# Kernel tuning notes

Measured on AMD Instinct MI355X. Metric: run time of the kernel, lower is better.

## Reference

```python
import jax, jax.numpy as jnp
import numpy as np

N_DRUG, N_DIS, E, D = 10000, 15000, 1048576, 128

def setup_inputs() -> dict:
    key = jax.random.key(0)
    k = jax.random.split(key, 6)
    return {
        "z_drug": jax.random.normal(k[0], (N_DRUG, D), dtype=jnp.float32),
        "z_disease": jax.random.normal(k[1], (N_DIS, D), dtype=jnp.float32),
        "row": jax.random.randint(k[2], (E,), 0, N_DRUG),
        "col": jax.random.randint(k[3], (E,), 0, N_DIS),
        "W1": jax.random.normal(k[4], (2 * D, D), dtype=jnp.float32) * (1.0 / np.sqrt(2 * D)),
        "b1": jnp.zeros((D,), dtype=jnp.float32),
        "W2": jax.random.normal(k[5], (D, 1), dtype=jnp.float32) * (1.0 / np.sqrt(D)),
        "b2": jnp.zeros((1,), dtype=jnp.float32),
    }

def reference(z_drug, z_disease, row, col, W1, b1, W2, b2):
    # gather per-edge embeddings and concatenate: [E, 2D]
    z = jnp.concatenate([z_drug[row], z_disease[col]], axis=-1)
    h = jax.nn.relu(z @ W1 + b1)          # [E, D]
    out = h @ W2 + b2                      # [E, 1]
    return out.reshape(-1)                 # [E]
```

## Files before the change

kernel.cpp:

```cpp
#include <hip/hip_runtime.h>

typedef __attribute__((ext_vector_type(8))) short short8;
typedef __attribute__((ext_vector_type(4))) float floatx4;
typedef _Float16 half8 __attribute__((ext_vector_type(8)));
typedef _Float16 half4 __attribute__((ext_vector_type(4)));
typedef _Float16 half2v __attribute__((ext_vector_type(2)));

static __device__ __forceinline__ unsigned short f2bf(float x) {
    unsigned int u = __builtin_bit_cast(unsigned int, x);
    unsigned int r = (u + 0x7FFFu + ((u >> 16) & 1u)) >> 16;
    return (unsigned short)r;
}

__global__ void prep_w1(const float* __restrict__ W1, unsigned short* __restrict__ w1t,
                        unsigned* __restrict__ gcur) {
    int i = blockIdx.x * 256 + threadIdx.x;
    int n = i >> 8;
    int k = i & 255;
    w1t[n * 256 + k] = f2bf(W1[k * 128 + n]);
    if (i < 16) gcur[i] = 0;
}

__global__ __launch_bounds__(256, 2) void mid_kernel(
    const float* __restrict__ zd, const float* __restrict__ zs,
    const unsigned short* __restrict__ w1t, const float* __restrict__ b1,
    _Float16* __restrict__ ud, _Float16* __restrict__ us,
    int ndrows, int nsrows, int ntd, int nbg,
    const int* __restrict__ row, const int* __restrict__ col,
    unsigned* __restrict__ gcur, unsigned* __restrict__ rcbuf,
    unsigned* __restrict__ eidbuf, int E)
{
    if ((int)blockIdx.x < nbg) {
        const int tid  = threadIdx.x;
        const int lane = tid & 63;
        const int wave = tid >> 6;
        const int wh   = wave >> 1;
        const int we   = wave & 1;
        const int l15  = lane & 15;
        const int quad = lane >> 4;

        const int b = blockIdx.x;
        const bool isD = (b < ntd);
        const float* __restrict__ z = isD ? zd : zs;
        _Float16* __restrict__ u = isD ? ud : us;
        const int nrows = isD ? ndrows : nsrows;
        const int m0    = (isD ? b : b - ntd) * 64;
        const int koff0 = isD ? 0 : 128;

        short8 wfrag[16];
        #pragma unroll
        for (int s = 0; s < 4; ++s)
            #pragma unroll
            for (int mt = 0; mt < 4; ++mt)
                wfrag[s * 4 + mt] = *reinterpret_cast<const short8*>(
                    &w1t[(size_t)(wh * 64 + mt * 16 + l15) * 256 + koff0 + s * 32 + quad * 8]);

        floatx4 acc[2][4];
        #pragma unroll
        for (int mt = 0; mt < 4; ++mt) {
            floatx4 bb = *reinterpret_cast<const floatx4*>(&b1[wh * 64 + mt * 16 + quad * 4]);
            bb *= 0.5f;
            acc[0][mt] = bb;
            acc[1][mt] = bb;
        }

        int rowi[2], rowc[2];
        #pragma unroll
        for (int et = 0; et < 2; ++et) {
            rowi[et] = m0 + we * 32 + et * 16 + l15;
            rowc[et] = rowi[et] < nrows ? rowi[et] : nrows - 1;
        }

        #pragma unroll
        for (int s = 0; s < 4; ++s) {
            short8 bf[2];
            #pragma unroll
            for (int et = 0; et < 2; ++et) {
                const float* src = &z[(size_t)rowc[et] * 128 + s * 32 + quad * 8];
                floatx4 lo = *reinterpret_cast<const floatx4*>(src);
                floatx4 hi = *reinterpret_cast<const floatx4*>(src + 4);
                short8 t;
                t[0] = (short)f2bf(lo[0]); t[1] = (short)f2bf(lo[1]);
                t[2] = (short)f2bf(lo[2]); t[3] = (short)f2bf(lo[3]);
                t[4] = (short)f2bf(hi[0]); t[5] = (short)f2bf(hi[1]);
                t[6] = (short)f2bf(hi[2]); t[7] = (short)f2bf(hi[3]);
                bf[et] = t;
            }
            #pragma unroll
            for (int et = 0; et < 2; ++et)
                #pragma unroll
                for (int mt = 0; mt < 4; ++mt)
                    acc[et][mt] = __builtin_amdgcn_mfma_f32_16x16x32_bf16(
                        wfrag[s * 4 + mt], bf[et], acc[et][mt], 0, 0, 0);
        }

        #pragma unroll
        for (int et = 0; et < 2; ++et) {
            if (rowi[et] < nrows) {
                #pragma unroll
                for (int mt = 0; mt < 4; ++mt) {
                    half4 hv;
                    #pragma unroll
                    for (int rr = 0; rr < 4; ++rr) hv[rr] = (_Float16)acc[et][mt][rr];
                    *reinterpret_cast<half4*>(
                        &u[(size_t)rowi[et] * 128 + wh * 64 + mt * 16 + quad * 4]) = hv;
                }
            }
        }
    } else {
        __shared__ unsigned wl[4][4];
        __shared__ unsigned gb[4];
        const int tid  = threadIdx.x;
        const int lane = tid & 63;
        const int wave = tid >> 6;
        const int sb   = blockIdx.x - nbg;
        const long base = (long)sb * 2048;

        unsigned rc[8], off[8];
        int cls0, cls1, cls2, cls3, cls4, cls5, cls6, cls7;
        unsigned w0 = 0, w1 = 0, w2c = 0, w3 = 0;

        #pragma unroll
        for (int k = 0; k < 8; ++k) {
            long e = base + wave * 512 + k * 64 + lane;
            int r = row[e], c = col[e];
            rc[k] = (unsigned)r | ((unsigned)c << 14);
            int cl = ((r >= 5000) ? 2 : 0) | ((c >= 7500) ? 1 : 0);
            unsigned long long m0 = __ballot(cl == 0);
            unsigned long long m1 = __ballot(cl == 1);
            unsigned long long m2 = __ballot(cl == 2);
            unsigned long long m3 = __ballot(cl == 3);
            unsigned long long mlt = (1ull << lane) - 1ull;
            unsigned long long mc = (cl == 0) ? m0 : (cl == 1) ? m1 : (cl == 2) ? m2 : m3;
            unsigned wb = (cl == 0) ? w0 : (cl == 1) ? w1 : (cl == 2) ? w2c : w3;
            off[k] = wb + (unsigned)__popcll(mc & mlt);
            w0 += (unsigned)__popcll(m0); w1 += (unsigned)__popcll(m1);
            w2c += (unsigned)__popcll(m2); w3 += (unsigned)__popcll(m3);
            switch (k) {
                case 0: cls0 = cl; break; case 1: cls1 = cl; break;
                case 2: cls2 = cl; break; case 3: cls3 = cl; break;
                case 4: cls4 = cl; break; case 5: cls5 = cl; break;
                case 6: cls6 = cl; break; default: cls7 = cl; break;
            }
        }
        if (lane < 4) {
            unsigned wv = (lane == 0) ? w0 : (lane == 1) ? w1 : (lane == 2) ? w2c : w3;
            wl[wave][lane] = wv;
        }
        __syncthreads();
        if (tid < 4) {
            unsigned tot = wl[0][tid] + wl[1][tid] + wl[2][tid] + wl[3][tid];
            gb[tid] = atomicAdd(&gcur[tid], tot);
        }
        __syncthreads();
        unsigned p0 = 0, p1 = 0, p2 = 0, p3 = 0;
        for (int w = 0; w < 4; ++w)
            if (w < wave) { p0 += wl[w][0]; p1 += wl[w][1]; p2 += wl[w][2]; p3 += wl[w][3]; }

        #pragma unroll
        for (int k = 0; k < 8; ++k) {
            long e = base + wave * 512 + k * 64 + lane;
            int cl = (k == 0) ? cls0 : (k == 1) ? cls1 : (k == 2) ? cls2 : (k == 3) ? cls3
                   : (k == 4) ? cls4 : (k == 5) ? cls5 : (k == 6) ? cls6 : cls7;
            unsigned pre = (cl == 0) ? p0 : (cl == 1) ? p1 : (cl == 2) ? p2 : p3;
            unsigned pos = gb[cl] + pre + off[k];
            rcbuf[(size_t)cl * E + pos]  = rc[k];
            eidbuf[(size_t)cl * E + pos] = (unsigned)e;
        }
    }
}

__global__ __launch_bounds__(256, 8) void edge_eval(
    const _Float16* __restrict__ ud, const _Float16* __restrict__ us,
    const unsigned* __restrict__ gcur, const unsigned* __restrict__ rcbuf,
    const unsigned* __restrict__ eidbuf,
    const float* __restrict__ w2, const float* __restrict__ b2,
    float* __restrict__ out, int E)
{
    const int tid  = threadIdx.x;
    const int lane = tid & 63;
    const int wave = tid >> 6;
    const int le   = lane >> 3;
    const int q    = lane & 7;
    const int lslot = wave * 8 + le;

    const int b    = blockIdx.x;
    const int xcd  = b & 7;
    const int cls  = xcd >> 1;
    const int sub  = ((b >> 3) << 1) | (xcd & 1);
    const int NSUB = (int)((gridDim.x >> 3) << 1);

    const unsigned n = gcur[cls];
    const int nch = (int)((n + 31u) >> 5);
    const unsigned* __restrict__ rcb = rcbuf + (size_t)cls * E;
    const unsigned* __restrict__ eib = eidbuf + (size_t)cls * E;

#if __has_builtin(__builtin_amdgcn_fdot2)
    half2v w2h[8];
    #pragma unroll
    for (int i = 0; i < 2; ++i)
        #pragma unroll
        for (int p = 0; p < 4; ++p) {
            half2v t;
            t[0] = (_Float16)w2[i * 64 + q * 8 + 2 * p];
            t[1] = (_Float16)w2[i * 64 + q * 8 + 2 * p + 1];
            w2h[i * 4 + p] = t;
        }
#else
    float w2r[16];
    #pragma unroll
    for (int i = 0; i < 2; ++i) {
        *reinterpret_cast<floatx4*>(&w2r[i * 8]) =
            *reinterpret_cast<const floatx4*>(&w2[i * 64 + q * 8]);
        *reinterpret_cast<floatx4*>(&w2r[i * 8 + 4]) =
            *reinterpret_cast<const floatx4*>(&w2[i * 64 + q * 8 + 4]);
    }
#endif
    const float b2v = b2[0];

    int t = sub;
    if (t >= nch) return;

    unsigned ei0 = (unsigned)t * 32u + (unsigned)lslot;
    bool v0 = ei0 < n;
    unsigned ci0 = v0 ? ei0 : 0u;
    unsigned rc0 = rcb[ci0];
    unsigned id0 = eib[ci0];

    while (true) {
        const int tn = t + NSUB;

        unsigned r = rc0 & 16383u, c = rc0 >> 14;
        const _Float16* up = ud + (size_t)r * 128 + q * 8;
        const _Float16* vp = us + (size_t)c * 128 + q * 8;
        half8 U0 = *reinterpret_cast<const half8*>(up);
        half8 U1 = *reinterpret_cast<const half8*>(up + 64);
        half8 V0 = *reinterpret_cast<const half8*>(vp);
        half8 V1 = *reinterpret_cast<const half8*>(vp + 64);

        unsigned rc1 = 0, id1 = 0;
        bool v1 = false;
        if (tn < nch) {
            unsigned ei1 = (unsigned)tn * 32u + (unsigned)lslot;
            v1 = ei1 < n;
            unsigned ci1 = v1 ? ei1 : 0u;
            rc1 = rcb[ci1];
            id1 = eib[ci1];
        }

        float acc = 0.f;
        half8 s0 = U0 + V0;
        s0 = __builtin_elementwise_max(s0, (half8)(_Float16)0.f);
        half8 s1 = U1 + V1;
        s1 = __builtin_elementwise_max(s1, (half8)(_Float16)0.f);
#if __has_builtin(__builtin_amdgcn_fdot2)
        #pragma unroll
        for (int p = 0; p < 4; ++p) {
            half2v pr0; pr0[0] = s0[2 * p]; pr0[1] = s0[2 * p + 1];
            acc = __builtin_amdgcn_fdot2(pr0, w2h[p], acc, false);
            half2v pr1; pr1[0] = s1[2 * p]; pr1[1] = s1[2 * p + 1];
            acc = __builtin_amdgcn_fdot2(pr1, w2h[4 + p], acc, false);
        }
#else
        #pragma unroll
        for (int j = 0; j < 8; ++j) {
            acc += (float)s0[j] * w2r[j];
            acc += (float)s1[j] * w2r[8 + j];
        }
#endif
        acc += __shfl_xor(acc, 1);
        acc += __shfl_xor(acc, 2);
        acc += __shfl_xor(acc, 4);
        if (v0 && q == 0) out[id0] = acc + b2v;

        if (tn >= nch) break;
        t = tn; rc0 = rc1; id0 = id1; v0 = v1;
    }
}

extern "C" void kernel_launch(void* const* d_in, const int* in_sizes, int n_in,
                              void* d_out, int out_size, void* d_ws, size_t ws_size,
                              hipStream_t stream) {
    const float* zd = (const float*)d_in[0];
    const float* zs = (const float*)d_in[1];
    const int*   row = (const int*)d_in[2];
    const int*   col = (const int*)d_in[3];
    const float* W1 = (const float*)d_in[4];
    const float* b1 = (const float*)d_in[5];
    const float* w2 = (const float*)d_in[6];
    const float* b2 = (const float*)d_in[7];
    float* out = (float*)d_out;

    const int nd = in_sizes[0];
    const int ns = in_sizes[1];
    const int E  = in_sizes[2];
    const int ndrows = nd / 128;
    const int nsrows = ns / 128;

    unsigned short* w1t = (unsigned short*)d_ws;
    _Float16* ud = (_Float16*)((char*)d_ws + 128 * 256 * sizeof(unsigned short));
    _Float16* us = ud + (size_t)ndrows * 128;
    size_t off = (size_t)((char*)(us + (size_t)nsrows * 128) - (char*)d_ws);
    off = (off + 63) & ~(size_t)63;
    unsigned* gcur   = (unsigned*)((char*)d_ws + off);
    unsigned* rcbuf  = gcur + 16;
    unsigned* eidbuf = rcbuf + (size_t)4 * E;

    hipLaunchKernelGGL(prep_w1, dim3(128), dim3(256), 0, stream, W1, w1t, gcur);

    const int ntd = (ndrows + 63) / 64;
    const int nts = (nsrows + 63) / 64;
    const int nbg = ntd + nts;
    const int nsb = E / 2048;
    hipLaunchKernelGGL(mid_kernel, dim3(nbg + nsb), dim3(256), 0, stream,
                       zd, zs, w1t, b1, ud, us, ndrows, nsrows, ntd, nbg,
                       row, col, gcur, rcbuf, eidbuf, E);

    hipLaunchKernelGGL(edge_eval, dim3(2048), dim3(256), 0, stream,
                       ud, us, gcur, rcbuf, eidbuf, w2, b2, out, E);
}
```

Baseline: 122.1 us.

## Fold W1 prep into mid kernel, pack edge records, deepen edge pipeline

Removes the separate W1 transpose/convert kernel: each GEMM block now reads W1 directly with strided loads and converts it to bf16 in registers, and the counters are zeroed with a memset. Row/col and edge id are packed into one 64-bit record so the bucketed edge list is written and read as a single stream. The edge kernel switches from strided chunk assignment to contiguous chunk ranges per block and software-pipelines two chunks at a time with records prefetched two ahead. Its grid drops to 1536 blocks with a launch-bound occupancy of 6. The risks are uncoalesced W1 reads repeated by every GEMM block and higher register pressure in the edge loop.

```diff
diff --git a/kernel.cpp b/kernel.cpp
--- a/kernel.cpp
+++ b/kernel.cpp
@@ -12,23 +12,13 @@
     return (unsigned short)r;
 }
 
-__global__ void prep_w1(const float* __restrict__ W1, unsigned short* __restrict__ w1t,
-                        unsigned* __restrict__ gcur) {
-    int i = blockIdx.x * 256 + threadIdx.x;
-    int n = i >> 8;
-    int k = i & 255;
-    w1t[n * 256 + k] = f2bf(W1[k * 128 + n]);
-    if (i < 16) gcur[i] = 0;
-}
-
 __global__ __launch_bounds__(256, 2) void mid_kernel(
     const float* __restrict__ zd, const float* __restrict__ zs,
-    const unsigned short* __restrict__ w1t, const float* __restrict__ b1,
+    const float* __restrict__ W1, const float* __restrict__ b1,
     _Float16* __restrict__ ud, _Float16* __restrict__ us,
     int ndrows, int nsrows, int ntd, int nbg,
     const int* __restrict__ row, const int* __restrict__ col,
-    unsigned* __restrict__ gcur, unsigned* __restrict__ rcbuf,
-    unsigned* __restrict__ eidbuf, int E)
+    unsigned* __restrict__ gcur, unsigned long long* __restrict__ recbuf, int E)
 {
     if ((int)blockIdx.x < nbg) {
         const int tid  = threadIdx.x;
@@ -46,19 +36,26 @@
         const int nrows = isD ? ndrows : nsrows;
         const int m0    = (isD ? b : b - ntd) * 64;
         const int koff0 = isD ? 0 : 128;
+        const int whbase = wh * 64;
 
         short8 wfrag[16];
         #pragma unroll
         for (int s = 0; s < 4; ++s)
             #pragma unroll
-            for (int mt = 0; mt < 4; ++mt)
-                wfrag[s * 4 + mt] = *reinterpret_cast<const short8*>(
-                    &w1t[(size_t)(wh * 64 + mt * 16 + l15) * 256 + koff0 + s * 32 + quad * 8]);
+            for (int mt = 0; mt < 4; ++mt) {
+                short8 t;
+                #pragma unroll
+                for (int j = 0; j < 8; ++j)
+                    t[j] = (short)f2bf(
+                        W1[(size_t)(koff0 + s * 32 + quad * 8 + j) * 128 +
+                           whbase + mt * 16 + l15]);
+                wfrag[s * 4 + mt] = t;
+            }
 
         floatx4 acc[2][4];
         #pragma unroll
         for (int mt = 0; mt < 4; ++mt) {
-            floatx4 bb = *reinterpret_cast<const floatx4*>(&b1[wh * 64 + mt * 16 + quad * 4]);
+            floatx4 bb = *reinterpret_cast<const floatx4*>(&b1[whbase + mt * 16 + quad * 4]);
             bb *= 0.5f;
             acc[0][mt] = bb;
             acc[1][mt] = bb;
@@ -103,7 +100,7 @@
                     #pragma unroll
                     for (int rr = 0; rr < 4; ++rr) hv[rr] = (_Float16)acc[et][mt][rr];
                     *reinterpret_cast<half4*>(
-                        &u[(size_t)rowi[et] * 128 + wh * 64 + mt * 16 + quad * 4]) = hv;
+                        &u[(size_t)rowi[et] * 128 + whbase + mt * 16 + quad * 4]) = hv;
                 }
             }
         }
@@ -164,16 +161,15 @@
                    : (k == 4) ? cls4 : (k == 5) ? cls5 : (k == 6) ? cls6 : cls7;
             unsigned pre = (cl == 0) ? p0 : (cl == 1) ? p1 : (cl == 2) ? p2 : p3;
             unsigned pos = gb[cl] + pre + off[k];
-            rcbuf[(size_t)cl * E + pos]  = rc[k];
-            eidbuf[(size_t)cl * E + pos] = (unsigned)e;
+            recbuf[(size_t)cl * E + pos] =
+                (unsigned long long)rc[k] | ((unsigned long long)(unsigned)e << 32);
         }
     }
 }
 
-__global__ __launch_bounds__(256, 8) void edge_eval(
+__global__ __launch_bounds__(256, 6) void edge_eval(
     const _Float16* __restrict__ ud, const _Float16* __restrict__ us,
-    const unsigned* __restrict__ gcur, const unsigned* __restrict__ rcbuf,
-    const unsigned* __restrict__ eidbuf,
+    const unsigned* __restrict__ gcur, const unsigned long long* __restrict__ recbuf,
     const float* __restrict__ w2, const float* __restrict__ b2,
     float* __restrict__ out, int E)
 {
@@ -185,15 +181,13 @@
     const int lslot = wave * 8 + le;
 
     const int b    = blockIdx.x;
-    const int xcd  = b & 7;
-    const int cls  = xcd >> 1;
-    const int sub  = ((b >> 3) << 1) | (xcd & 1);
+    const int cls  = (b & 7) >> 1;
+    const int sub  = ((b >> 3) << 1) | (b & 1);
     const int NSUB = (int)((gridDim.x >> 3) << 1);
 
     const unsigned n = gcur[cls];
     const int nch = (int)((n + 31u) >> 5);
-    const unsigned* __restrict__ rcb = rcbuf + (size_t)cls * E;
-    const unsigned* __restrict__ eib = eidbuf + (size_t)cls * E;
+    const unsigned long long* __restrict__ recb = recbuf + (size_t)cls * E;
 
 #if __has_builtin(__builtin_amdgcn_fdot2)
     half2v w2h[8];
@@ -218,64 +212,96 @@
 #endif
     const float b2v = b2[0];
 
-    int t = sub;
-    if (t >= nch) return;
-
-    unsigned ei0 = (unsigned)t * 32u + (unsigned)lslot;
-    bool v0 = ei0 < n;
-    unsigned ci0 = v0 ? ei0 : 0u;
-    unsigned rc0 = rcb[ci0];
-    unsigned id0 = eib[ci0];
-
+    const int K = (nch + NSUB - 1) / NSUB;
+    int t = sub * K;
+    int tend = t + K;
+    if (tend > nch) tend = nch;
+    if (t >= tend) return;
+
+#define LOADREC(RV, VV, tt)                                                    \
+    {                                                                          \
+        unsigned ei = (unsigned)(tt) * 32u + (unsigned)lslot;                  \
+        VV = ei < n;                                                           \
+        RV = recb[VV ? ei : 0u];                                               \
+    }
+
+#define GATHER(D, RV)                                                          \
+    {                                                                          \
+        unsigned r = (unsigned)(RV) & 16383u;                                  \
+        unsigned c = ((unsigned)(RV) >> 14) & 16383u;                          \
+        const _Float16* up = ud + (size_t)r * 128 + q * 8;                     \
+        const _Float16* vp = us + (size_t)c * 128 + q * 8;                     \
+        D[0] = *reinterpret_cast<const half8*>(up);                            \
+        D[1] = *reinterpret_cast<const half8*>(up + 64);                       \
+        D[2] = *reinterpret_cast<const half8*>(vp);                            \
+        D[3] = *reinterpret_cast<const half8*>(vp + 64);                       \
+    }
+
+#if __has_builtin(__builtin_amdgcn_fdot2)
+#define DOTBODY(D, accv)                                                       \
+    half8 s0 = D[0] + D[2];                                                    \
+    s0 = __builtin_elementwise_max(s0, (half8)(_Float16)0.f);                  \
+    half8 s1 = D[1] + D[3];                                                    \
+    s1 = __builtin_elementwise_max(s1, (half8)(_Float16)0.f);                  \
+    _Pragma("unroll")                                                          \
+    for (int p = 0; p < 4; ++p) {                                              \
+        half2v pr0; pr0[0] = s0[2 * p]; pr0[1] = s0[2 * p + 1];                \
+        accv = __builtin_amdgcn_fdot2(pr0, w2h[p], accv, false);               \
+        half2v pr1; pr1[0] = s1[2 * p]; pr1[1] = s1[2 * p + 1];                \
+        accv = __builtin_amdgcn_fdot2(pr1, w2h[4 + p], accv, false);           \
+    }
+#else
+#define DOTBODY(D, accv)                                                       \
+    half8 s0 = D[0] + D[2];                                                    \
+    s0 = __builtin_elementwise_max(s0, (half8)(_Float16)0.f);                  \
+    half8 s1 = D[1] + D[3];                                                    \
+    s1 = __builtin_elementwise_max(s1, (half8)(_Float16)0.f);                  \
+    _Pragma("unroll")                                                          \
+    for (int j = 0; j < 8; ++j) {                                              \
+        accv += (float)s0[j] * w2r[j];                                         \
+        accv += (float)s1[j] * w2r[8 + j];                                     \
+    }
+#endif
+
+#define COMPUTE(D, RV, VV)                                                     \
+    {                                                                          \
+        float acc = 0.f;                                                       \
+        DOTBODY(D, acc)                                                        \
+        acc += __shfl_xor(acc, 1);                                             \
+        acc += __shfl_xor(acc, 2);                                             \
+        acc += __shfl_xor(acc, 4);                                             \
+        if ((VV) && q == 0) out[(unsigned)((RV) >> 32)] = acc + b2v;           \
+    }
+
+    unsigned long long recA, recB = 0, recA2 = 0, recB2 = 0;
+    bool vA, vB = false, vA2 = false, vB2 = false;
+    LOADREC(recA, vA, t)
+    bool hasB = (t + 1 < tend);
+    if (hasB) LOADREC(recB, vB, t + 1)
+
+    half8 dA[4], dB[4];
     while (true) {
-        const int tn = t + NSUB;
-
-        unsigned r = rc0 & 16383u, c = rc0 >> 14;
-        const _Float16* up = ud + (size_t)r * 128 + q * 8;
-        const _Float16* vp = us + (size_t)c * 128 + q * 8;
-        half8 U0 = *reinterpret_cast<const half8*>(up);
-        half8 U1 = *reinterpret_cast<const half8*>(up + 64);
-        half8 V0 = *reinterpret_cast<const half8*>(vp);
-        half8 V1 = *reinterpret_cast<const half8*>(vp + 64);
-
-        unsigned rc1 = 0, id1 = 0;
-        bool v1 = false;
-        if (tn < nch) {
-            unsigned ei1 = (unsigned)tn * 32u + (unsigned)lslot;
-            v1 = ei1 < n;
-            unsigned ci1 = v1 ? ei1 : 0u;
-            rc1 = rcb[ci1];
-            id1 = eib[ci1];
-        }
-
-        float acc = 0.f;
-        half8 s0 = U0 + V0;
-        s0 = __builtin_elementwise_max(s0, (half8)(_Float16)0.f);
-        half8 s1 = U1 + V1;
-        s1 = __builtin_elementwise_max(s1, (half8)(_Float16)0.f);
-#if __has_builtin(__builtin_amdgcn_fdot2)
-        #pragma unroll
-        for (int p = 0; p < 4; ++p) {
-            half2v pr0; pr0[0] = s0[2 * p]; pr0[1] = s0[2 * p + 1];
-            acc = __builtin_amdgcn_fdot2(pr0, w2h[p], acc, false);
-            half2v pr1; pr1[0] = s1[2 * p]; pr1[1] = s1[2 * p + 1];
-            acc = __builtin_amdgcn_fdot2(pr1, w2h[4 + p], acc, false);
-        }
-#else
-        #pragma unroll
-        for (int j = 0; j < 8; ++j) {
-            acc += (float)s0[j] * w2r[j];
-            acc += (float)s1[j] * w2r[8 + j];
-        }
-#endif
-        acc += __shfl_xor(acc, 1);
-        acc += __shfl_xor(acc, 2);
-        acc += __shfl_xor(acc, 4);
-        if (v0 && q == 0) out[id0] = acc + b2v;
-
-        if (tn >= nch) break;
-        t = tn; rc0 = rc1; id0 = id1; v0 = v1;
-    }
+        GATHER(dA, recA)
+        if (hasB) GATHER(dB, recB)
+
+        bool hasA2 = (t + 2 < tend), hasB2 = (t + 3 < tend);
+        if (hasA2) LOADREC(recA2, vA2, t + 2)
+        if (hasB2) LOADREC(recB2, vB2, t + 3)
+
+        COMPUTE(dA, recA, vA)
+        if (!hasB) break;
+        COMPUTE(dB, recB, vB)
+
+        if (!hasA2) break;
+        recA = recA2; vA = vA2;
+        recB = recB2; vB = vB2;
+        hasB = hasB2;
+        t += 2;
+    }
+#undef LOADREC
+#undef GATHER
+#undef DOTBODY
+#undef COMPUTE
 }
 
 extern "C" void kernel_launch(void* const* d_in, const int* in_sizes, int n_in,
@@ -297,25 +323,23 @@
     const int ndrows = nd / 128;
     const int nsrows = ns / 128;
 
-    unsigned short* w1t = (unsigned short*)d_ws;
-    _Float16* ud = (_Float16*)((char*)d_ws + 128 * 256 * sizeof(unsigned short));
+    _Float16* ud = (_Float16*)d_ws;
     _Float16* us = ud + (size_t)ndrows * 128;
     size_t off = (size_t)((char*)(us + (size_t)nsrows * 128) - (char*)d_ws);
     off = (off + 63) & ~(size_t)63;
-    unsigned* gcur   = (unsigned*)((char*)d_ws + off);
-    unsigned* rcbuf  = gcur + 16;
-    unsigned* eidbuf = rcbuf + (size_t)4 * E;
-
-    hipLaunchKernelGGL(prep_w1, dim3(128), dim3(256), 0, stream, W1, w1t, gcur);
+    unsigned* gcur = (unsigned*)((char*)d_ws + off);
+    unsigned long long* recbuf = (unsigned long long*)((char*)gcur + 64);
+
+    hipMemsetAsync(gcur, 0, 16 * sizeof(unsigned), stream);
 
     const int ntd = (ndrows + 63) / 64;
     const int nts = (nsrows + 63) / 64;
     const int nbg = ntd + nts;
     const int nsb = E / 2048;
     hipLaunchKernelGGL(mid_kernel, dim3(nbg + nsb), dim3(256), 0, stream,
-                       zd, zs, w1t, b1, ud, us, ndrows, nsrows, ntd, nbg,
-                       row, col, gcur, rcbuf, eidbuf, E);
-
-    hipLaunchKernelGGL(edge_eval, dim3(2048), dim3(256), 0, stream,
-                       ud, us, gcur, rcbuf, eidbuf, w2, b2, out, E);
+                       zd, zs, W1, b1, ud, us, ndrows, nsrows, ntd, nbg,
+                       row, col, gcur, recbuf, E);
+
+    hipLaunchKernelGGL(edge_eval, dim3(1536), dim3(256), 0, stream,
+                       ud, us, gcur, recbuf, w2, b2, out, E);
 }
```

Result: no change. 123.7 us (+1.3%).
